# Performance work log

Measured on AMD Instinct MI355X. Metric: run time of the kernel, lower is better.

Reference implementation:

```python
import jax, jax.numpy as jnp
import numpy as np
from jax import lax

M_DIM = 128
L1 = L2 = L3 = L4 = 4
L = L1 * L2 * L3 * L4  # 256
RANK = 2
BATCH, D = 4, 16
W = D - RANK + 1  # 15 windows per dim (linear mode, stride 1, drop)


def _make_bbasis():
    # Bbasis[idx, i] = prod_d cos(2*pi*(j_d+1)/(i+2)), idx = ((j1*L2+j2)*L3+j3)*L4+j4
    i = jnp.arange(M_DIM, dtype=jnp.float32)
    def c(Ld):
        j = jnp.arange(D_ := Ld, dtype=jnp.float32)
        return jnp.cos(2.0 * jnp.pi * (j[:, None] + 1.0) / (i[None, :] + 2.0))  # (Ld, m)
    B1, B2, B3, B4 = c(L1), c(L2), c(L3), c(L4)
    Bb = (B1[:, None, None, None, :] * B2[None, :, None, None, :]
          * B3[None, None, :, None, :] * B4[None, None, None, :, :])
    return Bb.reshape(L, M_DIM).astype(jnp.float32)


def setup_inputs() -> dict:
    key = jax.random.key(0)
    k1, k2, k3 = jax.random.split(key, 3)
    vec_arr = jax.random.normal(k1, (BATCH, D, D, D, D, M_DIM), dtype=jnp.float32)
    # M initialized as identity + small noise (nn.init.eye_ is exactly eye; noise keeps grads non-trivial)
    M = jnp.eye(M_DIM, dtype=jnp.float32) + 0.01 * jax.random.normal(k2, (M_DIM, M_DIM), dtype=jnp.float32)
    Acoeff = jax.random.uniform(k3, (M_DIM, L), minval=-0.1, maxval=0.1, dtype=jnp.float32)
    Bbasis = _make_bbasis()
    return {"vec_arr": vec_arr, "M": M, "Acoeff": Acoeff, "Bbasis": Bbasis}


def _basis_index():
    # window coords k_d in [0, W), basis index uses j_d = k_d mod L_d
    k = jnp.arange(W)
    j1 = (k % L1)[:, None, None, None]
    j2 = (k % L2)[None, :, None, None]
    j3 = (k % L3)[None, None, :, None]
    j4 = (k % L4)[None, None, None, :]
    idx = ((j1 * L2 + j2) * L3 + j3) * L4 + j4  # (W,W,W,W)
    return idx.reshape(-1)  # (W^4,)


def reference(vec_arr, M, Acoeff, Bbasis):
    # 4D sliding-window mean (linear mode, stride 1, 'drop'), rank_op='avg'.
    # mean(window @ M.T) == mean(window) @ M.T (linearity), so pool then one GEMM.
    win = (1, RANK, RANK, RANK, RANK, 1)
    pooled = lax.reduce_window(vec_arr, jnp.float32(0.0), lax.add, win,
                               (1, 1, 1, 1, 1, 1), 'VALID') / float(RANK ** 4)
    # agg[b, k1..k4, j] = sum_i pooled[...,i] * M[j,i]  (i.e. x @ M.T)
    agg = jnp.einsum('bwxyzi,ji->bwxyzj', pooled, M)  # (B, W,W,W,W, m)
    agg = agg.reshape(agg.shape[0], -1, M_DIM)        # (B, W^4, m)
    idx = _basis_index()                               # (W^4,)
    # Position-dependent descriptor N(k) = Acoeff[:, idx] * Bbasis[idx, :]
    Nk = Acoeff.T[idx] * Bbasis[idx]                   # (W^4, m)
    return Nk[None, :, :] - agg                        # (B, W^4, m) deviation
```

## Files before the change

kernel.cpp:

```cpp
#include <hip/hip_runtime.h>
#include <hip/hip_bf16.h>
#include <stdint.h>

#define MD   128
#define LBAS 256

#define MBF_OFF 131072ull
#define WS_NEED (131072ull + 32768ull)

typedef __attribute__((ext_vector_type(8))) __bf16 bf16x8;
typedef __attribute__((ext_vector_type(4))) float floatx4;
typedef __attribute__((ext_vector_type(8))) unsigned short ushortx8;
typedef __attribute__((ext_vector_type(4))) unsigned short ushortx4;

__device__ __forceinline__ float bf2f(unsigned short u){
  union { unsigned int i; float f; } v; v.i = ((unsigned int)u) << 16; return v.f;
}
__device__ __forceinline__ unsigned short f2bf(float x){
  union { float f; unsigned int i; } v; v.f = x;
  unsigned int r = v.i + 0x7FFFu + ((v.i >> 16) & 1u);
  return (unsigned short)(r >> 16);
}
__device__ __forceinline__ int detect_f32(const void* Bbasis){
  return ((const unsigned int*)Bbasis)[0] == 0x3F800000u;
}

__global__ __launch_bounds__(256) void nk2_kernel(const void* __restrict__ Acoeff,
                                                  const void* __restrict__ Bbasis,
                                                  const void* __restrict__ Mmat,
                                                  float* __restrict__ NkFull,
                                                  unsigned short* __restrict__ Mbf){
  int gid = blockIdx.x * 256 + threadIdx.x;
  const int isf = detect_f32(Bbasis);
  if (gid < LBAS * MD){
    int idx = gid >> 7, j = gid & 127;
    float a, b;
    if (isf){ a = ((const float*)Acoeff)[j*LBAS+idx]; b = ((const float*)Bbasis)[idx*MD+j]; }
    else    { a = bf2f(((const unsigned short*)Acoeff)[j*LBAS+idx]);
              b = bf2f(((const unsigned short*)Bbasis)[idx*MD+j]); }
    NkFull[gid] = a * b;
  } else {
    int m = gid - LBAS * MD;
    if (m < MD * MD){
      Mbf[m] = isf ? f2bf(((const float*)Mmat)[m]) : ((const unsigned short*)Mmat)[m];
    }
  }
}

__global__ __launch_bounds__(256, 4) void mega_kernel(const void* __restrict__ vec,
                                                      const float* __restrict__ NkFull,
                                                      const unsigned short* __restrict__ Mbf,
                                                      const void* __restrict__ Bbasis,
                                                      void* __restrict__ out){
  __shared__ __align__(16) float S[32 * 132];
  __shared__ __align__(16) unsigned short pp[2][15][136];
  __shared__ __align__(16) unsigned short Ab[16 * 136];
  __shared__ __align__(16) float sNkStep[512];

  const int xcd  = blockIdx.x & 7;
  const int slot = blockIdx.x >> 3;
  const int b    = xcd >> 1;
  const int s    = slot * 2 + (xcd & 1);
  if (s >= 225) return;
  const int w3 = s / 15;
  const int w2 = s - w3 * 15;
  const int t  = threadIdx.x;
  const int isf = detect_f32(Bbasis);

  const int wave = t >> 6, lane = t & 63;
  const int quad = lane >> 4, l16 = lane & 15;

  const size_t vbase0 = (size_t)b * 8388608 + (size_t)w2 * 32768 + (size_t)w3 * 2048;

  int offF[4];
#pragma unroll
  for (int k = 0; k < 4; ++k){
    const int ci = k * 256 + t;
    const int row = ci >> 5;
    offF[k] = (row >> 4) * 2048 + (row & 15) * 128 + (ci & 31) * 4;
  }
  int offB[2];
#pragma unroll
  for (int k = 0; k < 2; ++k){
    const int ci = k * 256 + t;
    const int row = ci >> 4;
    offB[k] = (row >> 4) * 2048 + (row & 15) * 128 + (ci & 15) * 8;
  }

  floatx4 pre[4][2];

  if (isf){
    const float* vf = (const float*)vec + vbase0;
#pragma unroll
    for (int k = 0; k < 4; ++k){
      pre[k][0] = *(const floatx4*)(vf + offF[k]);
      pre[k][1] = *(const floatx4*)(vf + offF[k] + 32768);
    }
  } else {
    const unsigned short* vh = (const unsigned short*)vec + vbase0;
#pragma unroll
    for (int k = 0; k < 2; ++k){
      *(ushortx8*)&pre[k][0] = *(const ushortx8*)(vh + offB[k]);
      *(ushortx8*)&pre[k][1] = *(const ushortx8*)(vh + offB[k] + 32768);
    }
  }

  bf16x8 mfr[2][4];
#pragma unroll
  for (int cc = 0; cc < 2; ++cc)
#pragma unroll
    for (int s4 = 0; s4 < 4; ++s4)
      *(ushortx8*)&mfr[cc][s4] =
          *(const ushortx8*)(Mbf + ((wave * 2 + cc) * 16 + l16) * 128 + s4 * 32 + quad * 8);

  const int pw4 = t >> 4;
  const int pc8 = (t & 15) * 8;

  for (int x1 = 0; x1 < 16; ++x1){
    __syncthreads();

    if (isf){
#pragma unroll
      for (int k = 0; k < 4; ++k){
        const int ci = k * 256 + t;
        const int row = ci >> 5, c4 = (ci & 31) * 4;
        floatx4 sv;
#pragma unroll
        for (int q = 0; q < 4; ++q) sv[q] = pre[k][0][q] + pre[k][1][q];
        *(floatx4*)&S[row * 132 + c4] = sv;
      }
    } else {
#pragma unroll
      for (int k = 0; k < 2; ++k){
        const int ci = k * 256 + t;
        const int row = ci >> 4, c8 = (ci & 15) * 8;
        const ushortx8 a = *(const ushortx8*)&pre[k][0];
        const ushortx8 c = *(const ushortx8*)&pre[k][1];
#pragma unroll
        for (int q = 0; q < 8; ++q) S[row * 132 + c8 + q] = bf2f(a[q]) + bf2f(c[q]);
      }
    }

    if (x1 < 15){
      if (isf){
        const float* vf = (const float*)vec + vbase0 + (size_t)(x1 + 1) * 524288;
#pragma unroll
        for (int k = 0; k < 4; ++k){
          pre[k][0] = *(const floatx4*)(vf + offF[k]);
          pre[k][1] = *(const floatx4*)(vf + offF[k] + 32768);
        }
      } else {
        const unsigned short* vh = (const unsigned short*)vec + vbase0 + (size_t)(x1 + 1) * 524288;
#pragma unroll
        for (int k = 0; k < 2; ++k){
          *(ushortx8*)&pre[k][0] = *(const ushortx8*)(vh + offB[k]);
          *(ushortx8*)&pre[k][1] = *(const ushortx8*)(vh + offB[k] + 32768);
        }
      }
    }
    __syncthreads();

    const int cb = x1 & 1, pbuf = cb ^ 1;
    if (t < 240){
      float cur[8];
      const int p0 = pw4 * 132 + pc8;
#pragma unroll
      for (int e = 0; e < 8; ++e)
        cur[e] = ((S[p0 + e] + S[p0 + 132 + e]) +
                  (S[p0 + 16 * 132 + e] + S[p0 + 17 * 132 + e])) * 0.125f;
      ushortx8 cv;
#pragma unroll
      for (int e = 0; e < 8; ++e) cv[e] = f2bf(cur[e]);
      *(ushortx8*)&pp[cb][pw4][pc8] = cv;
      if (x1 > 0){
        const ushortx8 pv = *(const ushortx8*)&pp[pbuf][pw4][pc8];
        ushortx8 av;
#pragma unroll
        for (int e = 0; e < 8; ++e) av[e] = f2bf((cur[e] + bf2f(pv[e])) * 0.5f);
        *(ushortx8*)&Ab[pw4 * 136 + pc8] = av;
      }
    }
    __syncthreads();

    if (x1 > 0){
      floatx4 acc[2];
      acc[0] = (floatx4){0.f,0.f,0.f,0.f};
      acc[1] = (floatx4){0.f,0.f,0.f,0.f};
#pragma unroll
      for (int s4 = 0; s4 < 4; ++s4){
        const bf16x8 af = *(const bf16x8*)&Ab[l16 * 136 + s4 * 32 + quad * 8];
#pragma unroll
        for (int cc = 0; cc < 2; ++cc){
          acc[cc] = __builtin_amdgcn_mfma_f32_16x16x32_bf16(af, mfr[cc][s4], acc[cc], 0, 0, 0);
        }
      }
      float* Ct = S;
#pragma unroll
      for (int cc = 0; cc < 2; ++cc)
#pragma unroll
        for (int reg = 0; reg < 4; ++reg)
          Ct[(quad * 4 + reg) * 132 + (wave * 2 + cc) * 16 + l16] = acc[cc][reg];

      const int j1 = (x1 - 1) & 3;
      const int idxBase = ((j1 * 4 + (w2 & 3)) * 4 + (w3 & 3)) * 4;
#pragma unroll
      for (int k = 0; k < 2; ++k){
        const int e = k * 256 + t;
        sNkStep[e] = NkFull[(idxBase + (e >> 7)) * 128 + (e & 127)];
      }
      __syncthreads();

      const size_t outBase = ((size_t)(((b * 15 + (x1 - 1)) * 15 + w2) * 15 + w3)) * 15;
#pragma unroll
      for (int k = 0; k < 2; ++k){
        const int ci = k * 256 + t;
        if (ci < 480){
          const int row = ci >> 5, c4 = (ci & 31) * 4;
          const floatx4 v  = *(const floatx4*)&Ct[row * 132 + c4];
          const floatx4 nk = *(const floatx4*)&sNkStep[(row & 3) * 128 + c4];
          floatx4 o;
#pragma unroll
          for (int e = 0; e < 4; ++e) o[e] = nk[e] - v[e];
          if (isf){
            *(floatx4*)((float*)out + (outBase + row) * 128 + c4) = o;
          } else {
            ushortx4 ob;
#pragma unroll
            for (int e = 0; e < 4; ++e) ob[e] = f2bf(o[e]);
            *(ushortx4*)((unsigned short*)out + (outBase + row) * 128 + c4) = ob;
          }
        }
      }
    }
  }
}

extern "C" void kernel_launch(void* const* d_in, const int* in_sizes, int n_in,
                              void* d_out, int out_size, void* d_ws, size_t ws_size,
                              hipStream_t stream) {
  const void* vec = d_in[0];
  const void* Mm  = d_in[1];
  const void* Ac  = d_in[2];
  const void* Bb  = d_in[3];

  float* NkFull = (float*)d_ws;
  unsigned short* Mbf = (unsigned short*)((char*)d_ws + MBF_OFF);

  nk2_kernel<<<192, 256, 0, stream>>>(Ac, Bb, Mm, NkFull, Mbf);
  mega_kernel<<<904, 256, 0, stream>>>(vec, NkFull, Mbf, Bb, d_out);
}
```

Before: 245.8 us.

## Pool windows directly from registers and preload per-block Nk tile once

```diff
diff --git a/kernel.cpp b/kernel.cpp
--- a/kernel.cpp
+++ b/kernel.cpp
@@ -52,10 +52,10 @@
                                                       const unsigned short* __restrict__ Mbf,
                                                       const void* __restrict__ Bbasis,
                                                       void* __restrict__ out){
-  __shared__ __align__(16) float S[32 * 132];
+  __shared__ __align__(16) float Ct[16 * 132];
   __shared__ __align__(16) unsigned short pp[2][15][136];
   __shared__ __align__(16) unsigned short Ab[16 * 136];
-  __shared__ __align__(16) float sNkStep[512];
+  __shared__ __align__(16) float sNk[16 * 128];
 
   const int xcd  = blockIdx.x & 7;
   const int slot = blockIdx.x >> 3;
@@ -70,38 +70,34 @@
   const int wave = t >> 6, lane = t & 63;
   const int quad = lane >> 4, l16 = lane & 15;
 
+  const int pw4   = t >> 4;
+  const int pc8   = (t & 15) * 8;
+  const int owner = (t < 240);
+
   const size_t vbase0 = (size_t)b * 8388608 + (size_t)w2 * 32768 + (size_t)w3 * 2048;
 
-  int offF[4];
-#pragma unroll
-  for (int k = 0; k < 4; ++k){
-    const int ci = k * 256 + t;
-    const int row = ci >> 5;
-    offF[k] = (row >> 4) * 2048 + (row & 15) * 128 + (ci & 31) * 4;
-  }
-  int offB[2];
-#pragma unroll
-  for (int k = 0; k < 2; ++k){
-    const int ci = k * 256 + t;
-    const int row = ci >> 4;
-    offB[k] = (row >> 4) * 2048 + (row & 15) * 128 + (ci & 15) * 8;
-  }
-
-  floatx4 pre[4][2];
-
-  if (isf){
-    const float* vf = (const float*)vec + vbase0;
-#pragma unroll
-    for (int k = 0; k < 4; ++k){
-      pre[k][0] = *(const floatx4*)(vf + offF[k]);
-      pre[k][1] = *(const floatx4*)(vf + offF[k] + 32768);
-    }
-  } else {
-    const unsigned short* vh = (const unsigned short*)vec + vbase0;
-#pragma unroll
-    for (int k = 0; k < 2; ++k){
-      *(ushortx8*)&pre[k][0] = *(const ushortx8*)(vh + offB[k]);
-      *(ushortx8*)&pre[k][1] = *(const ushortx8*)(vh + offB[k] + 32768);
+  int offR[8];
+#pragma unroll
+  for (int r = 0; r < 8; ++r){
+    const int x2s = r >> 2, x3s = (r >> 1) & 1, e4 = r & 1;
+    offR[r] = x2s * 32768 + x3s * 2048 + (pw4 + e4) * 128 + pc8;
+  }
+
+  floatx4 pre[8][2];
+
+  if (owner){
+    if (isf){
+      const float* vf = (const float*)vec + vbase0;
+#pragma unroll
+      for (int r = 0; r < 8; ++r){
+        pre[r][0] = *(const floatx4*)(vf + offR[r]);
+        pre[r][1] = *(const floatx4*)(vf + offR[r] + 4);
+      }
+    } else {
+      const unsigned short* vh = (const unsigned short*)vec + vbase0;
+#pragma unroll
+      for (int r = 0; r < 8; ++r)
+        *(ushortx8*)&pre[r][0] = *(const ushortx8*)(vh + offR[r]);
     }
   }
 
@@ -113,61 +109,70 @@
       *(ushortx8*)&mfr[cc][s4] =
           *(const ushortx8*)(Mbf + ((wave * 2 + cc) * 16 + l16) * 128 + s4 * 32 + quad * 8);
 
-  const int pw4 = t >> 4;
-  const int pc8 = (t & 15) * 8;
+  {
+    const int j2f = (w2 & 3), j3f = (w3 & 3);
+#pragma unroll
+    for (int k = 0; k < 2; ++k){
+      const int ci = k * 256 + t;
+      const int row16 = ci >> 5, c4 = (ci & 31) * 4;
+      const int j1 = row16 >> 2, j4 = row16 & 3;
+      const int nkrow = ((j1 * 4 + j2f) * 4 + j3f) * 4 + j4;
+      *(floatx4*)&sNk[row16 * 128 + c4] = *(const floatx4*)&NkFull[nkrow * 128 + c4];
+    }
+  }
 
   for (int x1 = 0; x1 < 16; ++x1){
-    __syncthreads();
-
-    if (isf){
-#pragma unroll
-      for (int k = 0; k < 4; ++k){
-        const int ci = k * 256 + t;
-        const int row = ci >> 5, c4 = (ci & 31) * 4;
-        floatx4 sv;
-#pragma unroll
-        for (int q = 0; q < 4; ++q) sv[q] = pre[k][0][q] + pre[k][1][q];
-        *(floatx4*)&S[row * 132 + c4] = sv;
-      }
-    } else {
-#pragma unroll
-      for (int k = 0; k < 2; ++k){
-        const int ci = k * 256 + t;
-        const int row = ci >> 4, c8 = (ci & 15) * 8;
-        const ushortx8 a = *(const ushortx8*)&pre[k][0];
-        const ushortx8 c = *(const ushortx8*)&pre[k][1];
-#pragma unroll
-        for (int q = 0; q < 8; ++q) S[row * 132 + c8 + q] = bf2f(a[q]) + bf2f(c[q]);
-      }
-    }
-
-    if (x1 < 15){
+    const int cb = x1 & 1, pbuf = cb ^ 1;
+    float cur[8];
+    if (owner){
+      if (isf){
+#pragma unroll
+        for (int c = 0; c < 2; ++c){
+          const floatx4 s0a = pre[0][c] + pre[4][c];
+          const floatx4 s0b = pre[1][c] + pre[5][c];
+          const floatx4 s1a = pre[2][c] + pre[6][c];
+          const floatx4 s1b = pre[3][c] + pre[7][c];
+          const floatx4 cv4 = ((s0a + s0b) + (s1a + s1b)) * 0.125f;
+#pragma unroll
+          for (int e = 0; e < 4; ++e) cur[c * 4 + e] = cv4[e];
+        }
+      } else {
+        const ushortx8 b0 = *(const ushortx8*)&pre[0][0];
+        const ushortx8 b1 = *(const ushortx8*)&pre[1][0];
+        const ushortx8 b2 = *(const ushortx8*)&pre[2][0];
+        const ushortx8 b3 = *(const ushortx8*)&pre[3][0];
+        const ushortx8 b4 = *(const ushortx8*)&pre[4][0];
+        const ushortx8 b5 = *(const ushortx8*)&pre[5][0];
+        const ushortx8 b6 = *(const ushortx8*)&pre[6][0];
+        const ushortx8 b7 = *(const ushortx8*)&pre[7][0];
+#pragma unroll
+        for (int e = 0; e < 8; ++e){
+          const float s0a = bf2f(b0[e]) + bf2f(b4[e]);
+          const float s0b = bf2f(b1[e]) + bf2f(b5[e]);
+          const float s1a = bf2f(b2[e]) + bf2f(b6[e]);
+          const float s1b = bf2f(b3[e]) + bf2f(b7[e]);
+          cur[e] = ((s0a + s0b) + (s1a + s1b)) * 0.125f;
+        }
+      }
+    }
+
+    if (x1 < 15 && owner){
       if (isf){
         const float* vf = (const float*)vec + vbase0 + (size_t)(x1 + 1) * 524288;
 #pragma unroll
-        for (int k = 0; k < 4; ++k){
-          pre[k][0] = *(const floatx4*)(vf + offF[k]);
-          pre[k][1] = *(const floatx4*)(vf + offF[k] + 32768);
+        for (int r = 0; r < 8; ++r){
+          pre[r][0] = *(const floatx4*)(vf + offR[r]);
+          pre[r][1] = *(const floatx4*)(vf + offR[r] + 4);
         }
       } else {
         const unsigned short* vh = (const unsigned short*)vec + vbase0 + (size_t)(x1 + 1) * 524288;
 #pragma unroll
-        for (int k = 0; k < 2; ++k){
-          *(ushortx8*)&pre[k][0] = *(const ushortx8*)(vh + offB[k]);
-          *(ushortx8*)&pre[k][1] = *(const ushortx8*)(vh + offB[k] + 32768);
-        }
-      }
-    }
-    __syncthreads();
-
-    const int cb = x1 & 1, pbuf = cb ^ 1;
-    if (t < 240){
-      float cur[8];
-      const int p0 = pw4 * 132 + pc8;
-#pragma unroll
-      for (int e = 0; e < 8; ++e)
-        cur[e] = ((S[p0 + e] + S[p0 + 132 + e]) +
-                  (S[p0 + 16 * 132 + e] + S[p0 + 17 * 132 + e])) * 0.125f;
+        for (int r = 0; r < 8; ++r)
+          *(ushortx8*)&pre[r][0] = *(const ushortx8*)(vh + offR[r]);
+      }
+    }
+
+    if (owner){
       ushortx8 cv;
 #pragma unroll
       for (int e = 0; e < 8; ++e) cv[e] = f2bf(cur[e]);
@@ -194,22 +199,14 @@
           acc[cc] = __builtin_amdgcn_mfma_f32_16x16x32_bf16(af, mfr[cc][s4], acc[cc], 0, 0, 0);
         }
       }
-      float* Ct = S;
 #pragma unroll
       for (int cc = 0; cc < 2; ++cc)
 #pragma unroll
         for (int reg = 0; reg < 4; ++reg)
           Ct[(quad * 4 + reg) * 132 + (wave * 2 + cc) * 16 + l16] = acc[cc][reg];
-
-      const int j1 = (x1 - 1) & 3;
-      const int idxBase = ((j1 * 4 + (w2 & 3)) * 4 + (w3 & 3)) * 4;
-#pragma unroll
-      for (int k = 0; k < 2; ++k){
-        const int e = k * 256 + t;
-        sNkStep[e] = NkFull[(idxBase + (e >> 7)) * 128 + (e & 127)];
-      }
       __syncthreads();
 
+      const int j1sel = (x1 - 1) & 3;
       const size_t outBase = ((size_t)(((b * 15 + (x1 - 1)) * 15 + w2) * 15 + w3)) * 15;
 #pragma unroll
       for (int k = 0; k < 2; ++k){
@@ -217,7 +214,7 @@
         if (ci < 480){
           const int row = ci >> 5, c4 = (ci & 31) * 4;
           const floatx4 v  = *(const floatx4*)&Ct[row * 132 + c4];
-          const floatx4 nk = *(const floatx4*)&sNkStep[(row & 3) * 128 + c4];
+          const floatx4 nk = *(const floatx4*)&sNk[(j1sel * 4 + (row & 3)) * 128 + c4];
           floatx4 o;
 #pragma unroll
           for (int e = 0; e < 4; ++e) o[e] = nk[e] - v[e];
```

New measurement: 442.9 us. 1.8x slower.

## Keep pooled rows in registers, preload Nk once, store MFMA output directly

Applied to the files above, without the earlier changes.

```diff
diff --git a/kernel.cpp b/kernel.cpp
--- a/kernel.cpp
+++ b/kernel.cpp
@@ -53,9 +53,8 @@
                                                       const void* __restrict__ Bbasis,
                                                       void* __restrict__ out){
   __shared__ __align__(16) float S[32 * 132];
-  __shared__ __align__(16) unsigned short pp[2][15][136];
   __shared__ __align__(16) unsigned short Ab[16 * 136];
-  __shared__ __align__(16) float sNkStep[512];
+  __shared__ __align__(16) float sNk[16 * 128];
 
   const int xcd  = blockIdx.x & 7;
   const int slot = blockIdx.x >> 3;
@@ -113,8 +112,22 @@
       *(ushortx8*)&mfr[cc][s4] =
           *(const ushortx8*)(Mbf + ((wave * 2 + cc) * 16 + l16) * 128 + s4 * 32 + quad * 8);
 
+  {
+    const int j2f = (w2 & 3), j3f = (w3 & 3);
+#pragma unroll
+    for (int k = 0; k < 2; ++k){
+      const int ci = k * 256 + t;
+      const int row16 = ci >> 5, c4 = (ci & 31) * 4;
+      const int j1 = row16 >> 2, j4 = row16 & 3;
+      const int nkrow = ((j1 * 4 + j2f) * 4 + j3f) * 4 + j4;
+      *(floatx4*)&sNk[row16 * 128 + c4] = *(const floatx4*)&NkFull[nkrow * 128 + c4];
+    }
+  }
+
   const int pw4 = t >> 4;
   const int pc8 = (t & 15) * 8;
+  const int owner = (t < 240);
+  float prv[8];
 
   for (int x1 = 0; x1 < 16; ++x1){
     __syncthreads();
@@ -160,25 +173,21 @@
     }
     __syncthreads();
 
-    const int cb = x1 & 1, pbuf = cb ^ 1;
-    if (t < 240){
+    if (owner){
       float cur[8];
       const int p0 = pw4 * 132 + pc8;
 #pragma unroll
       for (int e = 0; e < 8; ++e)
         cur[e] = ((S[p0 + e] + S[p0 + 132 + e]) +
                   (S[p0 + 16 * 132 + e] + S[p0 + 17 * 132 + e])) * 0.125f;
-      ushortx8 cv;
-#pragma unroll
-      for (int e = 0; e < 8; ++e) cv[e] = f2bf(cur[e]);
-      *(ushortx8*)&pp[cb][pw4][pc8] = cv;
       if (x1 > 0){
-        const ushortx8 pv = *(const ushortx8*)&pp[pbuf][pw4][pc8];
         ushortx8 av;
 #pragma unroll
-        for (int e = 0; e < 8; ++e) av[e] = f2bf((cur[e] + bf2f(pv[e])) * 0.5f);
+        for (int e = 0; e < 8; ++e) av[e] = f2bf((cur[e] + prv[e]) * 0.5f);
         *(ushortx8*)&Ab[pw4 * 136 + pc8] = av;
       }
+#pragma unroll
+      for (int e = 0; e < 8; ++e) prv[e] = cur[e];
     }
     __syncthreads();
 
@@ -194,40 +203,24 @@
           acc[cc] = __builtin_amdgcn_mfma_f32_16x16x32_bf16(af, mfr[cc][s4], acc[cc], 0, 0, 0);
         }
       }
-      float* Ct = S;
-#pragma unroll
-      for (int cc = 0; cc < 2; ++cc)
-#pragma unroll
-        for (int reg = 0; reg < 4; ++reg)
-          Ct[(quad * 4 + reg) * 132 + (wave * 2 + cc) * 16 + l16] = acc[cc][reg];
-
-      const int j1 = (x1 - 1) & 3;
-      const int idxBase = ((j1 * 4 + (w2 & 3)) * 4 + (w3 & 3)) * 4;
-#pragma unroll
-      for (int k = 0; k < 2; ++k){
-        const int e = k * 256 + t;
-        sNkStep[e] = NkFull[(idxBase + (e >> 7)) * 128 + (e & 127)];
-      }
-      __syncthreads();
-
+
+      const int j1sel = (x1 - 1) & 3;
       const size_t outBase = ((size_t)(((b * 15 + (x1 - 1)) * 15 + w2) * 15 + w3)) * 15;
-#pragma unroll
-      for (int k = 0; k < 2; ++k){
-        const int ci = k * 256 + t;
-        if (ci < 480){
-          const int row = ci >> 5, c4 = (ci & 31) * 4;
-          const floatx4 v  = *(const floatx4*)&Ct[row * 132 + c4];
-          const floatx4 nk = *(const floatx4*)&sNkStep[(row & 3) * 128 + c4];
-          floatx4 o;
-#pragma unroll
-          for (int e = 0; e < 4; ++e) o[e] = nk[e] - v[e];
-          if (isf){
-            *(floatx4*)((float*)out + (outBase + row) * 128 + c4) = o;
-          } else {
-            ushortx4 ob;
-#pragma unroll
-            for (int e = 0; e < 4; ++e) ob[e] = f2bf(o[e]);
-            *(ushortx4*)((unsigned short*)out + (outBase + row) * 128 + c4) = ob;
+      const int col0 = wave * 32 + l16;
+#pragma unroll
+      for (int cc = 0; cc < 2; ++cc){
+        const int col = col0 + cc * 16;
+#pragma unroll
+        for (int reg = 0; reg < 4; ++reg){
+          const int row = quad * 4 + reg;
+          if (row < 15){
+            const float nk = sNk[(j1sel * 4 + (row & 3)) * 128 + col];
+            const float o = nk - acc[cc][reg];
+            if (isf){
+              ((float*)out)[(outBase + row) * 128 + col] = o;
+            } else {
+              ((unsigned short*)out)[(outBase + row) * 128 + col] = f2bf(o);
+            }
           }
         }
       }
```

New measurement: 261.7 us. +6.5%, slower.
